# Kernel optimization log

Hardware: AMD Instinct MI355X
Metric: run time of the kernel (lower is better)

Reference implementation:

```python
import jax, jax.numpy as jnp
import numpy as np

B, C, H, W = 16, 64, 256, 256
WS = 4  # window_size


def setup_inputs() -> dict:
    key = jax.random.key(0)
    k = jax.random.split(key, 5)
    c2, c4 = C // 2, C // 4
    return {
        "x": jax.random.normal(k[0], (B, C, H, W), dtype=jnp.float32),
        "w1": jax.random.normal(k[1], (c2, C), dtype=jnp.float32) * 0.05,
        "b1": jax.random.normal(k[2], (c2,), dtype=jnp.float32) * 0.05,
        "w2": jax.random.normal(k[3], (C, c4), dtype=jnp.float32) * 0.05,
        "b2": jax.random.normal(k[4], (C,), dtype=jnp.float32) * 0.05,
    }


def reference(x, w1, b1, w2, b2):
    b, c, h, w = x.shape
    ws = WS
    c2, c4 = c // 2, c // 4
    bnum = ws * ws                      # 16 windows positions
    l = (h // ws) * (w // ws)           # tokens per position

    # inp: 1x1 conv c->c/2 + ReLU
    x_ = jax.nn.relu(jnp.einsum('oc,bchw->bohw', w1, x) + b1[None, :, None, None])

    # rearrange 'b c (h dh) (w dw) -> b c (dh dw) (h w)', dh=dw=4
    qx = x_.reshape(b, c2, h // ws, ws, w // ws, ws)
    qx = qx.transpose(0, 1, 3, 5, 2, 4).reshape(b, c2, bnum, l)

    vx = qx[:, c4:]                     # [b, c/4, 16, l]

    # windowed mean + (buggy, faithful) 3rd moment: divisor is bnum (dim-2 size), not l
    mean = qx.mean(-1, keepdims=True)                    # [b, c/2, 16, 1]
    m3 = ((qx - mean) ** 3).sum(-1, keepdims=True) / bnum
    qkv = mean + m3

    q, v = qkv[:, :c4], qkv[:, c4:]     # each [b, c/4, 16, 1]

    atn = jax.nn.softmax(q @ jnp.swapaxes(q, -1, -2), axis=-1)  # [b, c/4, 16, 16]
    y = atn @ v                                                 # [b, c/4, 16, 1]

    Fv = vx * jax.nn.sigmoid(y)         # broadcast gate over l

    # inverse rearrange 'b c (dh dw) (h w) -> b c (h dh) (w dw)'
    Fv = Fv.reshape(b, c4, ws, ws, h // ws, w // ws)
    Fv = Fv.transpose(0, 1, 4, 2, 5, 3).reshape(b, c4, h, w)

    out = jnp.einsum('oc,bchw->bohw', w2, Fv) + b2[None, :, None, None]
    return out + x
```

## Files before the change

### kernel.cpp

```cpp
#include <hip/hip_runtime.h>

#define NB 16
#define NC 64
#define C2 32
#define C4 16
#define HH 256
#define WW 256
#define HW (HH*WW)


__global__ __launch_bounds__(256) void prep_kernel(const float* __restrict__ w1,
                                                   float* __restrict__ ws) {
    int t = threadIdx.x;
    for (int i = t; i < 24576; i += 256) ws[2048 + i] = 0.f;
    for (int i = t; i < 2048; i += 256) {
        int o = i >> 6, c = i & 63;
        ws[c * 32 + o] = w1[i];
    }
}

__device__ __forceinline__ void gl_lds16(const float* g, float* l) {
    __builtin_amdgcn_global_load_lds(
        (const __attribute__((address_space(1))) unsigned int*)g,
        (__attribute__((address_space(3))) unsigned int*)l,
        16, 0, 0);
}

__global__ __launch_bounds__(256) void stats_kernel(const float* __restrict__ x,
                                                    const float* __restrict__ w1t,
                                                    const float* __restrict__ b1,
                                                    float* __restrict__ stats) {
    __shared__ float lds[2][32 * 256];

    int b     = blockIdx.x >> 6;
    int sub   = blockIdx.x & 63;
    int r     = sub & 3;
    int chunk = sub >> 2;
    int t     = threadIdx.x;
    int wid   = t >> 6;
    int lane  = t & 63;
    const float* xb = x + (size_t)b * NC * HW;

#define STAGE(s_) do {                                                        \
        int i_ = (s_) >> 1;                                                   \
        int h_ = r + 4 * (chunk * 4 + i_);                                    \
        const float* gs_ = xb + (size_t)((s_) & 1) * 32 * HW + (size_t)h_ * WW; \
        float* ls_ = &lds[(s_) & 1][0];                                       \
        _Pragma("unroll")                                                     \
        for (int j_ = 0; j_ < 8; ++j_) {                                      \
            int cl_ = j_ * 4 + wid;                                           \
            gl_lds16(gs_ + (size_t)cl_ * HW + lane * 4, ls_ + cl_ * 256);     \
        }                                                                     \
    } while (0)

    float acc[32], S1[32], S2[32], S3[32];
    #pragma unroll
    for (int o = 0; o < 32; o++) { S1[o] = 0.f; S2[o] = 0.f; S3[o] = 0.f; }

    STAGE(0);
    for (int s = 0; s < 8; ++s) {
        if (s < 7) {
            STAGE(s + 1);
            asm volatile("s_waitcnt vmcnt(8)" ::: "memory");
        } else {
            asm volatile("s_waitcnt vmcnt(0)" ::: "memory");
        }
        __builtin_amdgcn_s_barrier();

        const float* L = &lds[s & 1][0];
        int cbase = (s & 1) * 32;
        if (cbase == 0) {
            #pragma unroll
            for (int o = 0; o < 32; o++) acc[o] = b1[o];
        }
        #pragma unroll 8
        for (int c = 0; c < 32; ++c) {
            float xc = L[c * 256 + t];
            #pragma unroll
            for (int o = 0; o < 32; o++) acc[o] += w1t[(cbase + c) * 32 + o] * xc;
        }
        if (cbase) {
            #pragma unroll
            for (int o = 0; o < 32; o++) {
                float v = acc[o] > 0.f ? acc[o] : 0.f;
                S1[o] += v;
                float p = v * v;
                S2[o] += p;
                S3[o] += p * v;
            }
        }
        __builtin_amdgcn_s_barrier();
    }
#undef STAGE

    #pragma unroll
    for (int o = 0; o < 32; o++) {
        float a = S1[o], bb = S2[o], cc = S3[o];
        #pragma unroll
        for (int m = 4; m <= 32; m <<= 1) {
            a  += __shfl_xor(a,  m);
            bb += __shfl_xor(bb, m);
            cc += __shfl_xor(cc, m);
        }
        if (lane < 4) {
            int si = r * 4 + lane;
            int idx = b * 512 + o * 16 + si;
            atomicAdd(&stats[idx],         a);
            atomicAdd(&stats[8192 + idx],  bb);
            atomicAdd(&stats[16384 + idx], cc);
        }
    }
}

__global__ __launch_bounds__(512) void attn_kernel(const float* __restrict__ stats,
                                                   float* __restrict__ gates) {
    int b = blockIdx.x;
    int t = threadIdx.x;
    __shared__ float qkv[512];
    {
        int idx = b * 512 + t;
        float S1 = stats[idx];
        float S2 = stats[8192 + idx];
        float S3 = stats[16384 + idx];
        float mu = S1 * (1.f / 4096.f);
        float m3 = (S3 - 3.f * mu * S2 + 2.f * 4096.f * mu * mu * mu) * (1.f / 16.f);
        qkv[t] = mu + m3;
    }
    __syncthreads();
    if (t < 256) {
        int o = t >> 4, s = t & 15;
        float qs = qkv[o * 16 + s];
        float mx = -1e30f;
        #pragma unroll
        for (int k = 0; k < 16; k++) mx = fmaxf(mx, qs * qkv[o * 16 + k]);
        float sum = 0.f, y = 0.f;
        #pragma unroll
        for (int k = 0; k < 16; k++) {
            float e = __expf(qs * qkv[o * 16 + k] - mx);
            sum += e;
            y   += e * qkv[(16 + o) * 16 + k];
        }
        y /= sum;
        float g = 1.f / (1.f + __expf(-y));
        gates[b * 256 + o * 16 + s] = g;
    }
}

__global__ __launch_bounds__(256) void out_kernel(const float* __restrict__ x,
                                                  const float* __restrict__ w1t,
                                                  const float* __restrict__ b1,
                                                  const float* __restrict__ w2,
                                                  const float* __restrict__ b2,
                                                  const float* __restrict__ gates,
                                                  float* __restrict__ out) {
    int bh = blockIdx.x;
    int b  = bh >> 8;
    int h  = bh & 255;
    int w  = threadIdx.x;
    int s  = (h & 3) * 4 + (w & 3);
    const float* xb = x   + (size_t)b * NC * HW + h * WW + w;
    float*       ob = out + (size_t)b * NC * HW + h * WW + w;

    __shared__ float gsh[256];
    gsh[w] = gates[b * 256 + w];
    __syncthreads();

    float xr[64];
    #pragma unroll
    for (int c = 0; c < 64; c++) xr[c] = xb[(size_t)c * HW];

    float fv[16];
    #pragma unroll
    for (int j = 0; j < 16; j++) fv[j] = b1[16 + j];
    #pragma unroll
    for (int c = 0; c < 64; c++) {
        float xc = xr[c];
        #pragma unroll
        for (int j = 0; j < 16; j++) fv[j] += w1t[c * 32 + 16 + j] * xc;
    }
    #pragma unroll
    for (int j = 0; j < 16; j++) {
        float v = fv[j] > 0.f ? fv[j] : 0.f;
        fv[j] = v * gsh[j * 16 + s];
    }
    #pragma unroll
    for (int o = 0; o < 64; o++) {
        float r = b2[o] + xr[o];
        #pragma unroll
        for (int j = 0; j < 16; j++) r += w2[o * 16 + j] * fv[j];
        ob[(size_t)o * HW] = r;
    }
}

extern "C" void kernel_launch(void* const* d_in, const int* in_sizes, int n_in,
                              void* d_out, int out_size, void* d_ws, size_t ws_size,
                              hipStream_t stream) {
    const float* x  = (const float*)d_in[0];
    const float* w1 = (const float*)d_in[1];
    const float* b1 = (const float*)d_in[2];
    const float* w2 = (const float*)d_in[3];
    const float* b2 = (const float*)d_in[4];
    float* ws    = (float*)d_ws;
    float* w1t   = ws;
    float* stats = ws + 2048;
    float* gates = ws + 26624;
    float* out   = (float*)d_out;

    prep_kernel <<<1,    256, 0, stream>>>(w1, ws);
    stats_kernel<<<1024, 256, 0, stream>>>(x, w1t, b1, stats);
    attn_kernel <<<16,   512, 0, stream>>>(stats, gates);
    out_kernel  <<<4096, 256, 0, stream>>>(x, w1t, b1, w2, b2, gates, out);
}
```

Baseline: 274.7 us.

## Split stats kernel work across waves by output-channel group with smaller column tiles

Restructures the stats kernel so each wave computes only 8 of the 32 hidden channels over a 64-column segment, instead of every thread computing all 32 channels. The grid doubles to 2048 blocks and each block loads all 64 input channels for a 64-wide row segment per stage. The intent is to cut per-thread register pressure (accumulators and S1/S2/S3 shrink from 32 to 8 each) to raise occupancy, and to keep weights wave-uniform via readfirstlane. In exchange, each x value is read from LDS by four waves, and there are more atomics and more blocks to schedule.

```diff
diff --git a/kernel.cpp b/kernel.cpp
--- a/kernel.cpp
+++ b/kernel.cpp
@@ -30,71 +30,77 @@
                                                     const float* __restrict__ w1t,
                                                     const float* __restrict__ b1,
                                                     float* __restrict__ stats) {
-    __shared__ float lds[2][32 * 256];
-
-    int b     = blockIdx.x >> 6;
-    int sub   = blockIdx.x & 63;
-    int r     = sub & 3;
-    int chunk = sub >> 2;
+    __shared__ float sbuf[2][64 * 64];
+
+    int bid   = blockIdx.x;
+    int b     = bid >> 7;
+    int rest  = bid & 127;
+    int r     = rest >> 5;
+    int rest2 = rest & 31;
+    int chunk = rest2 >> 2;
+    int colc  = rest2 & 3;
     int t     = threadIdx.x;
+    int lane  = t & 63;
     int wid   = t >> 6;
-    int lane  = t & 63;
-    const float* xb = x + (size_t)b * NC * HW;
-
-#define STAGE(s_) do {                                                        \
-        int i_ = (s_) >> 1;                                                   \
-        int h_ = r + 4 * (chunk * 4 + i_);                                    \
-        const float* gs_ = xb + (size_t)((s_) & 1) * 32 * HW + (size_t)h_ * WW; \
-        float* ls_ = &lds[(s_) & 1][0];                                       \
-        _Pragma("unroll")                                                     \
-        for (int j_ = 0; j_ < 8; ++j_) {                                      \
-            int cl_ = j_ * 4 + wid;                                           \
-            gl_lds16(gs_ + (size_t)cl_ * HW + lane * 4, ls_ + cl_ * 256);     \
-        }                                                                     \
+    int ogs   = __builtin_amdgcn_readfirstlane(wid);
+
+    const float* xseg = x + (size_t)b * NC * HW + colc * 64;
+    const float* wt   = w1t + ogs * 8;
+    float bias[8];
+    #pragma unroll
+    for (int o = 0; o < 8; o++) bias[o] = b1[ogs * 8 + o];
+
+#define STAGE(p_) do {                                                         \
+        int h_ = r + 4 * (chunk * 8 + (p_));                                   \
+        const float* gs_ = xseg + (size_t)h_ * WW;                             \
+        float* ls_ = &sbuf[(p_) & 1][0];                                       \
+        _Pragma("unroll")                                                      \
+        for (int k_ = 0; k_ < 4; ++k_) {                                       \
+            int c0_ = wid * 16 + k_ * 4;                                       \
+            gl_lds16(gs_ + (size_t)(c0_ + (lane >> 4)) * HW + (lane & 15) * 4, \
+                     ls_ + c0_ * 64);                                          \
+        }                                                                      \
     } while (0)
 
-    float acc[32], S1[32], S2[32], S3[32];
-    #pragma unroll
-    for (int o = 0; o < 32; o++) { S1[o] = 0.f; S2[o] = 0.f; S3[o] = 0.f; }
+    float S1[8], S2[8], S3[8];
+    #pragma unroll
+    for (int o = 0; o < 8; o++) { S1[o] = 0.f; S2[o] = 0.f; S3[o] = 0.f; }
 
     STAGE(0);
-    for (int s = 0; s < 8; ++s) {
-        if (s < 7) {
-            STAGE(s + 1);
-            asm volatile("s_waitcnt vmcnt(8)" ::: "memory");
+    #pragma unroll 1
+    for (int p = 0; p < 8; ++p) {
+        if (p < 7) {
+            STAGE(p + 1);
+            asm volatile("s_waitcnt vmcnt(4)" ::: "memory");
         } else {
             asm volatile("s_waitcnt vmcnt(0)" ::: "memory");
         }
         __builtin_amdgcn_s_barrier();
 
-        const float* L = &lds[s & 1][0];
-        int cbase = (s & 1) * 32;
-        if (cbase == 0) {
+        const float* L = &sbuf[p & 1][0];
+        float acc[8];
+        #pragma unroll
+        for (int o = 0; o < 8; o++) acc[o] = bias[o];
+        #pragma unroll
+        for (int c = 0; c < 64; ++c) {
+            float xc = L[c * 64 + lane];
             #pragma unroll
-            for (int o = 0; o < 32; o++) acc[o] = b1[o];
-        }
-        #pragma unroll 8
-        for (int c = 0; c < 32; ++c) {
-            float xc = L[c * 256 + t];
-            #pragma unroll
-            for (int o = 0; o < 32; o++) acc[o] += w1t[(cbase + c) * 32 + o] * xc;
-        }
-        if (cbase) {
-            #pragma unroll
-            for (int o = 0; o < 32; o++) {
-                float v = acc[o] > 0.f ? acc[o] : 0.f;
-                S1[o] += v;
-                float p = v * v;
-                S2[o] += p;
-                S3[o] += p * v;
-            }
+            for (int o = 0; o < 8; o++) acc[o] += wt[c * 32 + o] * xc;
+        }
+        #pragma unroll
+        for (int o = 0; o < 8; o++) {
+            float v = fmaxf(acc[o], 0.f);
+            float pw = v * v;
+            S1[o] += v;
+            S2[o] += pw;
+            S3[o] += pw * v;
         }
         __builtin_amdgcn_s_barrier();
     }
 #undef STAGE
 
     #pragma unroll
-    for (int o = 0; o < 32; o++) {
+    for (int o = 0; o < 8; o++) {
         float a = S1[o], bb = S2[o], cc = S3[o];
         #pragma unroll
         for (int m = 4; m <= 32; m <<= 1) {
@@ -103,8 +109,7 @@
             cc += __shfl_xor(cc, m);
         }
         if (lane < 4) {
-            int si = r * 4 + lane;
-            int idx = b * 512 + o * 16 + si;
+            int idx = b * 512 + (ogs * 8 + o) * 16 + r * 4 + lane;
             atomicAdd(&stats[idx],         a);
             atomicAdd(&stats[8192 + idx],  bb);
             atomicAdd(&stats[16384 + idx], cc);
@@ -207,7 +212,7 @@
     float* out   = (float*)d_out;
 
     prep_kernel <<<1,    256, 0, stream>>>(w1, ws);
-    stats_kernel<<<1024, 256, 0, stream>>>(x, w1t, b1, stats);
+    stats_kernel<<<2048, 256, 0, stream>>>(x, w1t, b1, stats);
     attn_kernel <<<16,   512, 0, stream>>>(stats, gates);
     out_kernel  <<<4096, 256, 0, stream>>>(x, w1t, b1, w2, b2, gates, out);
 }
```

New measurement: 231.7 us. -15.7%, faster.
